# Optimization experiments

Measured on AMD Instinct MI355X. Metric: run time of the kernel, lower is better.

The kernel has to match this reference:

```python
import jax, jax.numpy as jnp
import numpy as np

B, CIN, H, W = 16, 32, 256, 256
COUT, KH, KW = 32, 3, 3
NUM_EXPERTS = 8
PAD = ((1, 1), (1, 1))  # static 'same' padding for 3x3, stride 1, dilation 1


def setup_inputs() -> dict:
    key = jax.random.key(0)
    k_x, k_r, k_w, k_b = jax.random.split(key, 4)
    x = jax.random.normal(k_x, (B, CIN, H, W), dtype=jnp.float32)
    # routing weights are typically sigmoid/softmax outputs in [0,1]
    routing_weights = jax.nn.softmax(jax.random.normal(k_r, (B, NUM_EXPERTS), dtype=jnp.float32), axis=-1)
    num_params = COUT * CIN * KH * KW  # groups=1 -> in_channels//groups = CIN
    expert_weight = jax.random.normal(k_w, (NUM_EXPERTS, num_params), dtype=jnp.float32) * 0.05
    expert_bias = jax.random.normal(k_b, (NUM_EXPERTS, COUT), dtype=jnp.float32) * 0.05
    return {"x": x, "routing_weights": routing_weights,
            "expert_weight": expert_weight, "expert_bias": expert_bias}


def reference(x, routing_weights, expert_weight, expert_bias):
    b = x.shape[0]
    # Per-sample kernels: [B, num_params] -> [B, COUT, CIN, KH, KW]
    w = jnp.matmul(routing_weights, expert_weight).reshape(b, COUT, CIN, KH, KW)
    bias = jnp.matmul(routing_weights, expert_bias)  # [B, COUT]

    def conv_one(xi, wi):
        # xi: [CIN, H, W], wi: [COUT, CIN, KH, KW]
        return jax.lax.conv_general_dilated(
            xi[None], wi, window_strides=(1, 1), padding=PAD,
            dimension_numbers=("NCHW", "OIHW", "NCHW"))[0]

    out = jax.vmap(conv_one)(x, w)  # [B, COUT, H, W]
    out = out + bias[:, :, None, None]
    return out
```

## Files before the change

kernel.cpp:

```cpp
#include <hip/hip_runtime.h>

#define B_   16
#define CIN  32
#define COUT 32
#define HH   256
#define WW   256
#define NE   8
#define NTAP 9
#define KTOT (NTAP * CIN)

#define TH 8
#define TW 64
#define LROWS (TH + 2)
#define LCOLS (TW + 2)
#define PXS   40

typedef __attribute__((ext_vector_type(8))) short  short8;
typedef __attribute__((ext_vector_type(4))) float  floatx4;

__device__ __forceinline__ unsigned short f2bf(float f) {
    unsigned int u = __float_as_uint(f);
    u += 0x7FFFu + ((u >> 16) & 1u);
    return (unsigned short)(u >> 16);
}

__global__ __launch_bounds__(256) void prep_weights(
    const float* __restrict__ routing,
    const float* __restrict__ ew,
    const float* __restrict__ eb,
    unsigned short* __restrict__ ws_w,
    float* __restrict__ ws_b)
{
    const int b = blockIdx.x;
    const int t = threadIdx.x;
    float r[NE];
#pragma unroll
    for (int e = 0; e < NE; ++e) r[e] = routing[b * NE + e];

    for (int idx = t; idx < COUT * KTOT; idx += 256) {
        const int co  = idx / KTOT;
        const int k   = idx - co * KTOT;
        const int tap = k >> 5;
        const int ci  = k & 31;
        float acc = 0.f;
#pragma unroll
        for (int e = 0; e < NE; ++e)
            acc += r[e] * ew[e * (COUT * CIN * 9) + co * (CIN * 9) + ci * 9 + tap];
        ws_w[(b * COUT + co) * KTOT + k] = f2bf(acc);
    }
    if (t < COUT) {
        float acc = 0.f;
#pragma unroll
        for (int e = 0; e < NE; ++e) acc += r[e] * eb[e * COUT + t];
        ws_b[b * COUT + t] = acc;
    }
}

__global__ __launch_bounds__(256) void condconv_mfma(
    const float* __restrict__ x,
    const unsigned short* __restrict__ wsw,
    const float* __restrict__ wsb,
    float* __restrict__ out)
{
    __shared__ __align__(16) unsigned short s_x[LROWS * LCOLS * PXS];

    const int b    = blockIdx.z;
    const int x0   = blockIdx.x * TW;
    const int y0   = blockIdx.y * TH;
    const int t    = threadIdx.x;
    const int lane = t & 63;
    const int wv   = t >> 6;
    const int ln   = lane & 15;
    const int quad = lane >> 4;

    short8 afrag[NTAP][2];
    {
        const unsigned short* wb = wsw + (size_t)b * COUT * KTOT;
#pragma unroll
        for (int tap = 0; tap < NTAP; ++tap)
#pragma unroll
            for (int h = 0; h < 2; ++h)
                afrag[tap][h] = *(const short8*)(wb + (h * 16 + ln) * KTOT + tap * 32 + quad * 8);
    }
    float bias_v[2][4];
#pragma unroll
    for (int h = 0; h < 2; ++h)
#pragma unroll
        for (int rg = 0; rg < 4; ++rg)
            bias_v[h][rg] = wsb[b * COUT + h * 16 + quad * 4 + rg];

    for (int task = t; task < LROWS * LCOLS * 4; task += 256) {
        const int p   = task >> 2;
        const int c   = task & 3;
        const int row = p / LCOLS;
        const int col = p - row * LCOLS;
        const int gy  = y0 + row - 1;
        const int gx  = x0 + col - 1;
        short8 pk;
        if (gy >= 0 && gy < HH && gx >= 0 && gx < WW) {
            const float* src = x + (((size_t)b * CIN + c * 8) * HH + gy) * WW + gx;
#pragma unroll
            for (int u = 0; u < 8; ++u)
                pk[u] = (short)f2bf(src[(size_t)u * HH * WW]);
        } else {
#pragma unroll
            for (int u = 0; u < 8; ++u) pk[u] = 0;
        }
        *(short8*)&s_x[p * PXS + c * 8] = pk;
    }
    __syncthreads();

    floatx4 acc[8][2];
#pragma unroll
    for (int tt = 0; tt < 8; ++tt)
#pragma unroll
        for (int h = 0; h < 2; ++h)
            acc[tt][h] = (floatx4){0.f, 0.f, 0.f, 0.f};

#pragma unroll
    for (int tap = 0; tap < NTAP; ++tap) {
        const int dy = tap / 3;
        const int dx = tap - dy * 3;
#pragma unroll
        for (int tt = 0; tt < 8; ++tt) {
            const int r    = 2 * wv + (tt >> 2);
            const int q    = tt & 3;
            const int lrow = r + dy;
            const int lcol = q * 16 + ln + dx;
            const short8 bfr = *(const short8*)&s_x[(lrow * LCOLS + lcol) * PXS + quad * 8];
            acc[tt][0] = __builtin_amdgcn_mfma_f32_16x16x32_bf16(afrag[tap][0], bfr, acc[tt][0], 0, 0, 0);
            acc[tt][1] = __builtin_amdgcn_mfma_f32_16x16x32_bf16(afrag[tap][1], bfr, acc[tt][1], 0, 0, 0);
        }
    }

#pragma unroll
    for (int tt = 0; tt < 8; ++tt) {
        const int r  = 2 * wv + (tt >> 2);
        const int q  = tt & 3;
        const int gy = y0 + r;
        const int gx = x0 + q * 16 + ln;
#pragma unroll
        for (int h = 0; h < 2; ++h)
#pragma unroll
            for (int rg = 0; rg < 4; ++rg) {
                const int co = h * 16 + quad * 4 + rg;
                out[(((size_t)b * COUT + co) * HH + gy) * WW + gx] = acc[tt][h][rg] + bias_v[h][rg];
            }
    }
}

extern "C" void kernel_launch(void* const* d_in, const int* in_sizes, int n_in,
                              void* d_out, int out_size, void* d_ws, size_t ws_size,
                              hipStream_t stream) {
    const float* x       = (const float*)d_in[0];
    const float* routing = (const float*)d_in[1];
    const float* ew      = (const float*)d_in[2];
    const float* eb      = (const float*)d_in[3];
    float* out = (float*)d_out;

    unsigned short* ws_w = (unsigned short*)d_ws;
    float* ws_b = (float*)((char*)d_ws + (size_t)B_ * COUT * KTOT * 2);

    prep_weights<<<dim3(B_), dim3(256), 0, stream>>>(routing, ew, eb, ws_w, ws_b);

    dim3 grid(WW / TW, HH / TH, B_);
    condconv_mfma<<<grid, dim3(256), 0, stream>>>(x, ws_w, ws_b, out);
}
```

Baseline: 274.8 us.

## Vectorize halo loads, halve conv tile width, parallelize weight prep

The halo tile load now reads float4 groups of four columns per channel and converts them to bf16, replacing scalar loads. Tile width drops from 64 to 32 so there are twice as many blocks, with fewer accumulators per thread and a launch_bounds occupancy hint. The tile load is moved ahead of the weight-fragment loads so their latencies can overlap. Weight prep now spreads its work over 577 blocks instead of 16. The cost is more halo overhead per output and some redundant edge handling.

```diff
diff --git a/kernel.cpp b/kernel.cpp
--- a/kernel.cpp
+++ b/kernel.cpp
@@ -10,10 +10,11 @@
 #define KTOT (NTAP * CIN)
 
 #define TH 8
-#define TW 64
+#define TW 32
 #define LROWS (TH + 2)
 #define LCOLS (TW + 2)
 #define PXS   40
+#define NG    10
 
 typedef __attribute__((ext_vector_type(8))) short  short8;
 typedef __attribute__((ext_vector_type(4))) float  floatx4;
@@ -31,32 +32,35 @@
     unsigned short* __restrict__ ws_w,
     float* __restrict__ ws_b)
 {
-    const int b = blockIdx.x;
     const int t = threadIdx.x;
-    float r[NE];
-#pragma unroll
-    for (int e = 0; e < NE; ++e) r[e] = routing[b * NE + e];
-
-    for (int idx = t; idx < COUT * KTOT; idx += 256) {
-        const int co  = idx / KTOT;
-        const int k   = idx - co * KTOT;
-        const int tap = k >> 5;
-        const int ci  = k & 31;
+    if (blockIdx.x < 576) {
+        const int gidx = blockIdx.x * 256 + t;
+        const int b    = gidx / (COUT * KTOT);
+        const int rem  = gidx - b * (COUT * KTOT);
+        const int co   = rem / KTOT;
+        const int k    = rem - co * KTOT;
+        const int tap  = k >> 5;
+        const int ci   = k & 31;
         float acc = 0.f;
 #pragma unroll
         for (int e = 0; e < NE; ++e)
-            acc += r[e] * ew[e * (COUT * CIN * 9) + co * (CIN * 9) + ci * 9 + tap];
-        ws_w[(b * COUT + co) * KTOT + k] = f2bf(acc);
-    }
-    if (t < COUT) {
-        float acc = 0.f;
-#pragma unroll
-        for (int e = 0; e < NE; ++e) acc += r[e] * eb[e * COUT + t];
-        ws_b[b * COUT + t] = acc;
-    }
-}
-
-__global__ __launch_bounds__(256) void condconv_mfma(
+            acc += routing[b * NE + e] *
+                   ew[e * (COUT * CIN * 9) + co * (CIN * 9) + ci * 9 + tap];
+        ws_w[gidx] = f2bf(acc);
+    } else {
+        for (int i = t; i < B_ * COUT; i += 256) {
+            const int b  = i >> 5;
+            const int co = i & 31;
+            float acc = 0.f;
+#pragma unroll
+            for (int e = 0; e < NE; ++e)
+                acc += routing[b * NE + e] * eb[e * COUT + co];
+            ws_b[i] = acc;
+        }
+    }
+}
+
+__global__ __launch_bounds__(256, 4) void condconv_mfma(
     const float* __restrict__ x,
     const unsigned short* __restrict__ wsw,
     const float* __restrict__ wsb,
@@ -73,6 +77,53 @@
     const int ln   = lane & 15;
     const int quad = lane >> 4;
 
+    for (int task = t; task < LROWS * NG * 4; task += 256) {
+        const int c   = task & 3;
+        const int p   = task >> 2;
+        const int row = p / NG;
+        const int g   = p - row * NG;
+        const int gy  = y0 + row - 1;
+        const int gx0 = x0 + 4 * g - 4;
+        const bool iny = (gy >= 0) && (gy < HH);
+        if (iny && gx0 >= 0 && gx0 + 3 < WW) {
+            const float* src = x + (((size_t)(b * CIN + c * 8)) * HH + gy) * WW + gx0;
+            float4 v[8];
+#pragma unroll
+            for (int u = 0; u < 8; ++u)
+                v[u] = *(const float4*)(src + (size_t)u * HH * WW);
+#pragma unroll
+            for (int j = 0; j < 4; ++j) {
+                const int col = 4 * g - 3 + j;
+                if (col >= 0 && col < LCOLS) {
+                    short8 pk;
+#pragma unroll
+                    for (int u = 0; u < 8; ++u)
+                        pk[u] = (short)f2bf(((const float*)&v[u])[j]);
+                    *(short8*)&s_x[(row * LCOLS + col) * PXS + c * 8] = pk;
+                }
+            }
+        } else {
+#pragma unroll
+            for (int j = 0; j < 4; ++j) {
+                const int col = 4 * g - 3 + j;
+                if (col >= 0 && col < LCOLS) {
+                    const int gx = gx0 + j;
+                    short8 pk;
+                    if (iny && gx >= 0 && gx < WW) {
+                        const float* src = x + (((size_t)(b * CIN + c * 8)) * HH + gy) * WW + gx;
+#pragma unroll
+                        for (int u = 0; u < 8; ++u)
+                            pk[u] = (short)f2bf(src[(size_t)u * HH * WW]);
+                    } else {
+#pragma unroll
+                        for (int u = 0; u < 8; ++u) pk[u] = 0;
+                    }
+                    *(short8*)&s_x[(row * LCOLS + col) * PXS + c * 8] = pk;
+                }
+            }
+        }
+    }
+
     short8 afrag[NTAP][2];
     {
         const unsigned short* wb = wsw + (size_t)b * COUT * KTOT;
@@ -89,30 +140,11 @@
         for (int rg = 0; rg < 4; ++rg)
             bias_v[h][rg] = wsb[b * COUT + h * 16 + quad * 4 + rg];
 
-    for (int task = t; task < LROWS * LCOLS * 4; task += 256) {
-        const int p   = task >> 2;
-        const int c   = task & 3;
-        const int row = p / LCOLS;
-        const int col = p - row * LCOLS;
-        const int gy  = y0 + row - 1;
-        const int gx  = x0 + col - 1;
-        short8 pk;
-        if (gy >= 0 && gy < HH && gx >= 0 && gx < WW) {
-            const float* src = x + (((size_t)b * CIN + c * 8) * HH + gy) * WW + gx;
-#pragma unroll
-            for (int u = 0; u < 8; ++u)
-                pk[u] = (short)f2bf(src[(size_t)u * HH * WW]);
-        } else {
-#pragma unroll
-            for (int u = 0; u < 8; ++u) pk[u] = 0;
-        }
-        *(short8*)&s_x[p * PXS + c * 8] = pk;
-    }
     __syncthreads();
 
-    floatx4 acc[8][2];
-#pragma unroll
-    for (int tt = 0; tt < 8; ++tt)
+    floatx4 acc[4][2];
+#pragma unroll
+    for (int tt = 0; tt < 4; ++tt)
 #pragma unroll
         for (int h = 0; h < 2; ++h)
             acc[tt][h] = (floatx4){0.f, 0.f, 0.f, 0.f};
@@ -122,9 +154,9 @@
         const int dy = tap / 3;
         const int dx = tap - dy * 3;
 #pragma unroll
-        for (int tt = 0; tt < 8; ++tt) {
-            const int r    = 2 * wv + (tt >> 2);
-            const int q    = tt & 3;
+        for (int tt = 0; tt < 4; ++tt) {
+            const int r    = 2 * wv + (tt >> 1);
+            const int q    = tt & 1;
             const int lrow = r + dy;
             const int lcol = q * 16 + ln + dx;
             const short8 bfr = *(const short8*)&s_x[(lrow * LCOLS + lcol) * PXS + quad * 8];
@@ -134,9 +166,9 @@
     }
 
 #pragma unroll
-    for (int tt = 0; tt < 8; ++tt) {
-        const int r  = 2 * wv + (tt >> 2);
-        const int q  = tt & 3;
+    for (int tt = 0; tt < 4; ++tt) {
+        const int r  = 2 * wv + (tt >> 1);
+        const int q  = tt & 1;
         const int gy = y0 + r;
         const int gx = x0 + q * 16 + ln;
 #pragma unroll
@@ -161,7 +193,7 @@
     unsigned short* ws_w = (unsigned short*)d_ws;
     float* ws_b = (float*)((char*)d_ws + (size_t)B_ * COUT * KTOT * 2);
 
-    prep_weights<<<dim3(B_), dim3(256), 0, stream>>>(routing, ew, eb, ws_w, ws_b);
+    prep_weights<<<dim3(577), dim3(256), 0, stream>>>(routing, ew, eb, ws_w, ws_b);
 
     dim3 grid(WW / TW, HH / TH, B_);
     condconv_mfma<<<grid, dim3(256), 0, stream>>>(x, ws_w, ws_b, out);
```

New measurement: 301.3 us. 9.6% more time.
